# Performance work log

Hardware: AMD Instinct MI355X
Metric: run time of the kernel (lower is better)

## Reference

```python
import jax, jax.numpy as jnp
import numpy as np

STEPS_PER_PIECE = 4  # fixed-step RK4 substeps per spline piece (stands in for the adaptive solver)


def setup_inputs() -> dict:
    key = jax.random.key(0)
    ks = jax.random.split(key, 10)
    B, P, C, H, O = 4096, 64, 128, 128, 10  # batch, spline pieces, channels(=latent), hidden, output
    rn = lambda k, sh: jax.random.normal(k, sh, dtype=jnp.float32)
    return {
        "z0": rn(ks[0], (B, C)),
        # Hermite-cubic spline coefficients per piece: X(s) = a + b s + c s^2 + d s^3
        "coeffs": rn(ks[1], (B, P, C, 4)) * 0.05,
        "W1": rn(ks[2], (C, H)) / np.sqrt(C).astype(np.float32),
        "b1": jnp.zeros((H,), jnp.float32),
        "W2": rn(ks[3], (H, H)) / np.sqrt(H).astype(np.float32),
        "b2": jnp.zeros((H,), jnp.float32),
        "W3": rn(ks[4], (H, C)) / np.sqrt(H).astype(np.float32),
        "b3": jnp.zeros((C,), jnp.float32),
        "Wr": rn(ks[5], (H, O)) / np.sqrt(H).astype(np.float32),
        "br": jnp.zeros((O,), jnp.float32),
    }


def reference(z0, coeffs, W1, b1, W2, b2, W3, b3, Wr, br):
    P = coeffs.shape[1]
    n_steps = P * STEPS_PER_PIECE
    dt = jnp.float32(1.0 / STEPS_PER_PIECE)  # spline piece i covers t in [i, i+1]

    def dXdt(t):
        # derivative of the cubic spline at scalar time t -> [B, C]
        idx = jnp.clip(jnp.floor(t).astype(jnp.int32), 0, P - 1)
        s = t - idx.astype(t.dtype)
        c = jax.lax.dynamic_index_in_dim(coeffs, idx, axis=1, keepdims=False)  # [B, C, 4]
        return c[..., 1] + (2.0 * c[..., 2] + 3.0 * c[..., 3] * s) * s

    def f(z):
        # CDEFunc: Linear -> ELU -> Linear -> ReLU -> Linear
        h = jax.nn.elu(z @ W1 + b1)
        h = jax.nn.relu(h @ W2 + b2)
        return h @ W3 + b3

    def rk4_step(z, t):
        k1 = f(z) * dXdt(t)
        k2 = f(z + 0.5 * dt * k1) * dXdt(t + 0.5 * dt)
        k3 = f(z + 0.5 * dt * k2) * dXdt(t + 0.5 * dt)
        k4 = f(z + dt * k3) * dXdt(t + dt)
        z = z + (dt / 6.0) * (k1 + 2.0 * k2 + 2.0 * k3 + k4)
        return z, None

    ts = jnp.arange(n_steps, dtype=jnp.float32) * dt
    zT, _ = jax.lax.scan(rk4_step, z0, ts)  # terminal latent state = zt[:, 1]
    return zT @ Wr + br
```

## Files before the change

kernel.cpp:

```cpp
#include <hip/hip_runtime.h>
#include <hip/hip_bf16.h>
#include <math.h>


typedef short bf16x8 __attribute__((ext_vector_type(8)));
typedef float f32x4  __attribute__((ext_vector_type(4)));
typedef unsigned int u32x2 __attribute__((ext_vector_type(2)));

#define MFMA16(a, b, c) __builtin_amdgcn_mfma_f32_16x16x32_bf16((a), (b), (c), 0, 0, 0)

__device__ __forceinline__ unsigned short f2bf(float x) {
  unsigned int u = __float_as_uint(x);
  u += 0x7FFFu + ((u >> 16) & 1u);
  return (unsigned short)(u >> 16);
}

__device__ __forceinline__ unsigned int cvt_pk(float lo, float hi) {
  unsigned int r;
  asm("v_cvt_pk_bf16_f32 %0, %1, %2" : "=v"(r) : "v"(lo), "v"(hi));
  return r;
}

__device__ __forceinline__ void barrier_lgkm() {
  asm volatile("s_waitcnt lgkmcnt(0)" ::: "memory");
  __builtin_amdgcn_s_barrier();
  asm volatile("" ::: "memory");
}

__global__ __launch_bounds__(512, 2) void cde_fused(
    const float* __restrict__ z0, const float* __restrict__ coeffs,
    const float* __restrict__ W1, const float* __restrict__ b1,
    const float* __restrict__ W2, const float* __restrict__ b2,
    const float* __restrict__ W3, const float* __restrict__ b3,
    const float* __restrict__ Wr, const float* __restrict__ br,
    float* __restrict__ out) {
  __shared__ __align__(16) unsigned short zbuf[2][16][136];
  char* const lds = (char*)&zbuf[0][0][0];

  const int tid  = (int)threadIdx.x;
  const int lane = tid & 63;
  const int wv   = tid >> 6;
  const int l15  = lane & 15;
  const int q    = lane >> 4;
  const int n16  = wv * 16 + l15;
  const int nb4  = wv * 16 + q * 4;
  const int row0 = (int)blockIdx.x * 16;

  const int rdbyte = l15 * 272 + q * 16;
  const int wrbyte = l15 * 272 + nb4 * 2;

  bf16x8 wf1[4], wf2[4], wf3[4];
#pragma unroll
  for (int ks = 0; ks < 4; ++ks) {
    bf16x8 fa, fb, fc;
#pragma unroll
    for (int i = 0; i < 8; ++i) {
      const int k = ks * 32 + q * 8 + i;
      fa[i] = (short)f2bf(W1[k * 128 + n16]);
      fb[i] = (short)f2bf(W2[k * 128 + n16]);
      fc[i] = (short)f2bf(W3[k * 128 + n16]);
    }
    wf1[ks] = fa; wf2[ks] = fb; wf3[ks] = fc;
  }
  const f32x4 bv1 = *(const f32x4*)(b1 + nb4);
  const f32x4 bv2 = *(const f32x4*)(b2 + nb4);
  const f32x4 bv3 = *(const f32x4*)(b3 + nb4);

  f32x4 cf[4];
  auto coeff_load = [&](int p) {
    const float* cb = coeffs + ((size_t)(row0 + l15) * 64 + p) * 512 + nb4 * 4;
#pragma unroll
    for (int r = 0; r < 4; ++r) cf[r] = *(const f32x4*)(cb + r * 4);
  };
  float c1v[4], c2b[4], c3b[4];
  auto coeff_adopt = [&]() {
#pragma unroll
    for (int r = 0; r < 4; ++r) {
      c1v[r] = cf[r][1]; c2b[r] = 2.f * cf[r][2]; c3b[r] = 3.f * cf[r][3];
    }
  };

  auto stv = [&](int wb, const f32x4 v) {
    u32x2 w;
    w[0] = cvt_pk(v[0], v[1]);
    w[1] = cvt_pk(v[2], v[3]);
    *(u32x2*)(lds + (wb * 4352 + wrbyte)) = w;
  };

  float zr[4];
  {
    const f32x4 z = *(const f32x4*)(z0 + (size_t)(row0 + l15) * 128 + nb4);
#pragma unroll
    for (int r = 0; r < 4; ++r) zr[r] = z[r];
  }
  coeff_load(0);
  coeff_adopt();
  stv(0, f32x4{zr[0], zr[1], zr[2], zr[3]});
  barrier_lgkm();

  float kx[4], sacc[4], dxb[4];

  auto layer = [&](const bf16x8(&wf)[4], const f32x4 bias, int rb) -> f32x4 {
    const char* base = lds + rb * 4352 + rdbyte;
    bf16x8 x0 = *(const bf16x8*)(base);
    bf16x8 x1 = *(const bf16x8*)(base + 64);
    bf16x8 x2 = *(const bf16x8*)(base + 128);
    bf16x8 x3 = *(const bf16x8*)(base + 192);
    f32x4 Aa = {0.f, 0.f, 0.f, 0.f}, Ab = bias;
    Aa = MFMA16(wf[0], x0, Aa); Ab = MFMA16(wf[1], x1, Ab);
    Aa = MFMA16(wf[2], x2, Aa); Ab = MFMA16(wf[3], x3, Ab);
    return Aa + Ab;
  };

  auto run_f = [&](int sp) {
    f32x4 A = layer(wf1, bv1, sp);
    f32x4 h;
#pragma unroll
    for (int r = 0; r < 4; ++r) {
      const float v = A[r];
      h[r] = fmaxf(v, __expf(fminf(v, 0.f)) - 1.f);
    }
    stv(sp ^ 1, h);
    barrier_lgkm();
    A = layer(wf2, bv2, sp ^ 1);
#pragma unroll
    for (int r = 0; r < 4; ++r) h[r] = fmaxf(A[r], 0.f);
    stv(sp, h);
    barrier_lgkm();
    A = layer(wf3, bv3, sp);
#pragma unroll
    for (int r = 0; r < 4; ++r) kx[r] = A[r];
  };

#pragma unroll 1
  for (int p = 0; p < 64; ++p) {
    const bool pre = p < 63;
    if (pre) coeff_load(p + 1);

#pragma unroll
    for (int sub = 0; sub < 4; ++sub) {
      const float s0 = 0.25f * (float)sub;

      run_f(0);
      {
        f32x4 h;
#pragma unroll
        for (int r = 0; r < 4; ++r) {
          const float dx = c1v[r] + (c2b[r] + c3b[r] * s0) * s0;
          kx[r] *= dx; sacc[r] = kx[r];
          h[r] = zr[r] + 0.125f * kx[r];
        }
        stv(1, h);
      }
      barrier_lgkm();

      run_f(1);
      {
        const float sb = s0 + 0.125f;
        f32x4 h;
#pragma unroll
        for (int r = 0; r < 4; ++r) {
          dxb[r] = c1v[r] + (c2b[r] + c3b[r] * sb) * sb;
          kx[r] *= dxb[r]; sacc[r] += 2.f * kx[r];
          h[r] = zr[r] + 0.125f * kx[r];
        }
        stv(0, h);
      }
      barrier_lgkm();

      run_f(0);
      {
        f32x4 h;
#pragma unroll
        for (int r = 0; r < 4; ++r) {
          kx[r] *= dxb[r]; sacc[r] += 2.f * kx[r];
          h[r] = zr[r] + 0.25f * kx[r];
        }
        stv(1, h);
      }
      barrier_lgkm();

      run_f(1);
      if (sub == 3) {
        if (pre) {
#pragma unroll
          for (int r = 0; r < 4; ++r) kx[r] *= cf[r][1];
        } else {
#pragma unroll
          for (int r = 0; r < 4; ++r) kx[r] *= (c1v[r] + c2b[r] + c3b[r]);
        }
      } else {
        const float sc = s0 + 0.25f;
#pragma unroll
        for (int r = 0; r < 4; ++r)
          kx[r] *= c1v[r] + (c2b[r] + c3b[r] * sc) * sc;
      }
      {
        f32x4 h;
#pragma unroll
        for (int r = 0; r < 4; ++r) {
          sacc[r] += kx[r];
          zr[r] += (0.25f / 6.f) * sacc[r];
          h[r] = zr[r];
        }
        stv(0, h);
      }
      barrier_lgkm();
    }
    if (pre) coeff_adopt();
  }

  {
    float* zf = (float*)lds;
    *(f32x4*)(zf + l15 * 132 + nb4) = f32x4{zr[0], zr[1], zr[2], zr[3]};
  }
  barrier_lgkm();
  if (tid < 160) {
    const int row = tid / 10, o = tid - row * 10;
    const float* zf = (const float*)lds;
    float acc = br[o];
#pragma unroll 4
    for (int ch = 0; ch < 128; ++ch)
      acc = fmaf(zf[row * 132 + ch], Wr[ch * 10 + o], acc);
    out[(size_t)(row0 + row) * 10 + o] = acc;
  }
}

extern "C" void kernel_launch(void* const* d_in, const int* in_sizes, int n_in,
                              void* d_out, int out_size, void* d_ws, size_t ws_size,
                              hipStream_t stream) {
  const float* z0     = (const float*)d_in[0];
  const float* coeffs = (const float*)d_in[1];
  const float* W1 = (const float*)d_in[2]; const float* b1 = (const float*)d_in[3];
  const float* W2 = (const float*)d_in[4]; const float* b2 = (const float*)d_in[5];
  const float* W3 = (const float*)d_in[6]; const float* b3 = (const float*)d_in[7];
  const float* Wr = (const float*)d_in[8]; const float* br = (const float*)d_in[9];
  hipLaunchKernelGGL(cde_fused, dim3(256), dim3(512), 0, stream,
                     z0, coeffs, W1, b1, W2, b2, W3, b3, Wr, br, (float*)d_out);
}
```

Baseline: 823.4 us.

## Halve block to 4 waves, each computing two 16-column output tiles

Each wave now owns 32 output columns (two MFMA N-tiles) instead of 16, so the block shrinks from 8 to 4 waves. This halves the waves that take part in each of the many per-layer barriers, and each LDS activation fragment loaded feeds two MFMA chains, which raises instruction-level parallelism per wave. In exchange, per-wave register use doubles for weights and state. With 256 blocks on the GPU there may also be less latency hiding per CU.

```diff
diff --git a/kernel.cpp b/kernel.cpp
--- a/kernel.cpp
+++ b/kernel.cpp
@@ -27,7 +27,7 @@
   asm volatile("" ::: "memory");
 }
 
-__global__ __launch_bounds__(512, 2) void cde_fused(
+__global__ __launch_bounds__(256, 1) void cde_fused(
     const float* __restrict__ z0, const float* __restrict__ coeffs,
     const float* __restrict__ W1, const float* __restrict__ b1,
     const float* __restrict__ W2, const float* __restrict__ b2,
@@ -42,94 +42,118 @@
   const int wv   = tid >> 6;
   const int l15  = lane & 15;
   const int q    = lane >> 4;
-  const int n16  = wv * 16 + l15;
-  const int nb4  = wv * 16 + q * 4;
+  const int cb0  = wv * 32;
   const int row0 = (int)blockIdx.x * 16;
 
   const int rdbyte = l15 * 272 + q * 16;
-  const int wrbyte = l15 * 272 + nb4 * 2;
-
-  bf16x8 wf1[4], wf2[4], wf3[4];
-#pragma unroll
-  for (int ks = 0; ks < 4; ++ks) {
-    bf16x8 fa, fb, fc;
-#pragma unroll
-    for (int i = 0; i < 8; ++i) {
-      const int k = ks * 32 + q * 8 + i;
-      fa[i] = (short)f2bf(W1[k * 128 + n16]);
-      fb[i] = (short)f2bf(W2[k * 128 + n16]);
-      fc[i] = (short)f2bf(W3[k * 128 + n16]);
-    }
-    wf1[ks] = fa; wf2[ks] = fb; wf3[ks] = fc;
-  }
-  const f32x4 bv1 = *(const f32x4*)(b1 + nb4);
-  const f32x4 bv2 = *(const f32x4*)(b2 + nb4);
-  const f32x4 bv3 = *(const f32x4*)(b3 + nb4);
-
-  f32x4 cf[4];
+  const int wrbyte0 = l15 * 272 + (cb0 + 4 * q) * 2;
+  const int wrbyte1 = wrbyte0 + 32;
+
+  bf16x8 wf1[2][4], wf2[2][4], wf3[2][4];
+#pragma unroll
+  for (int mt = 0; mt < 2; ++mt) {
+    const int col = cb0 + 16 * mt + l15;
+#pragma unroll
+    for (int ks = 0; ks < 4; ++ks) {
+      bf16x8 fa, fb, fc;
+#pragma unroll
+      for (int i = 0; i < 8; ++i) {
+        const int k = ks * 32 + q * 8 + i;
+        fa[i] = (short)f2bf(W1[k * 128 + col]);
+        fb[i] = (short)f2bf(W2[k * 128 + col]);
+        fc[i] = (short)f2bf(W3[k * 128 + col]);
+      }
+      wf1[mt][ks] = fa; wf2[mt][ks] = fb; wf3[mt][ks] = fc;
+    }
+  }
+  f32x4 bv1[2], bv2[2], bv3[2];
+#pragma unroll
+  for (int mt = 0; mt < 2; ++mt) {
+    bv1[mt] = *(const f32x4*)(b1 + cb0 + 16 * mt + 4 * q);
+    bv2[mt] = *(const f32x4*)(b2 + cb0 + 16 * mt + 4 * q);
+    bv3[mt] = *(const f32x4*)(b3 + cb0 + 16 * mt + 4 * q);
+  }
+
+  f32x4 cf[8];
   auto coeff_load = [&](int p) {
-    const float* cb = coeffs + ((size_t)(row0 + l15) * 64 + p) * 512 + nb4 * 4;
-#pragma unroll
-    for (int r = 0; r < 4; ++r) cf[r] = *(const f32x4*)(cb + r * 4);
-  };
-  float c1v[4], c2b[4], c3b[4];
+    const float* cb = coeffs + ((size_t)(row0 + l15) * 64 + p) * 512;
+#pragma unroll
+    for (int mt = 0; mt < 2; ++mt)
+#pragma unroll
+      for (int r = 0; r < 4; ++r)
+        cf[mt * 4 + r] = *(const f32x4*)(cb + (cb0 + 16 * mt + 4 * q + r) * 4);
+  };
+  float c1v[8], c2b[8], c3b[8];
   auto coeff_adopt = [&]() {
 #pragma unroll
-    for (int r = 0; r < 4; ++r) {
-      c1v[r] = cf[r][1]; c2b[r] = 2.f * cf[r][2]; c3b[r] = 3.f * cf[r][3];
-    }
-  };
-
-  auto stv = [&](int wb, const f32x4 v) {
-    u32x2 w;
-    w[0] = cvt_pk(v[0], v[1]);
-    w[1] = cvt_pk(v[2], v[3]);
-    *(u32x2*)(lds + (wb * 4352 + wrbyte)) = w;
-  };
-
-  float zr[4];
+    for (int e = 0; e < 8; ++e) {
+      c1v[e] = cf[e][1]; c2b[e] = 2.f * cf[e][2]; c3b[e] = 3.f * cf[e][3];
+    }
+  };
+
+  auto stv = [&](int wb, const float (&h)[8]) {
+    u32x2 w0, w1;
+    w0[0] = cvt_pk(h[0], h[1]); w0[1] = cvt_pk(h[2], h[3]);
+    w1[0] = cvt_pk(h[4], h[5]); w1[1] = cvt_pk(h[6], h[7]);
+    *(u32x2*)(lds + (wb * 4352 + wrbyte0)) = w0;
+    *(u32x2*)(lds + (wb * 4352 + wrbyte1)) = w1;
+  };
+
+  float zr[8];
   {
-    const f32x4 z = *(const f32x4*)(z0 + (size_t)(row0 + l15) * 128 + nb4);
-#pragma unroll
-    for (int r = 0; r < 4; ++r) zr[r] = z[r];
+    const float* zp = z0 + (size_t)(row0 + l15) * 128;
+    const f32x4 za = *(const f32x4*)(zp + cb0 + 4 * q);
+    const f32x4 zb = *(const f32x4*)(zp + cb0 + 16 + 4 * q);
+#pragma unroll
+    for (int r = 0; r < 4; ++r) { zr[r] = za[r]; zr[4 + r] = zb[r]; }
   }
   coeff_load(0);
   coeff_adopt();
-  stv(0, f32x4{zr[0], zr[1], zr[2], zr[3]});
+  {
+    float h[8];
+#pragma unroll
+    for (int e = 0; e < 8; ++e) h[e] = zr[e];
+    stv(0, h);
+  }
   barrier_lgkm();
 
-  float kx[4], sacc[4], dxb[4];
-
-  auto layer = [&](const bf16x8(&wf)[4], const f32x4 bias, int rb) -> f32x4 {
+  float kx[8], sacc[8], dxb[8];
+
+  auto layer = [&](const bf16x8(&wf)[2][4], const f32x4(&bias)[2], int rb,
+                   f32x4& A0, f32x4& A1) {
     const char* base = lds + rb * 4352 + rdbyte;
     bf16x8 x0 = *(const bf16x8*)(base);
     bf16x8 x1 = *(const bf16x8*)(base + 64);
     bf16x8 x2 = *(const bf16x8*)(base + 128);
     bf16x8 x3 = *(const bf16x8*)(base + 192);
-    f32x4 Aa = {0.f, 0.f, 0.f, 0.f}, Ab = bias;
-    Aa = MFMA16(wf[0], x0, Aa); Ab = MFMA16(wf[1], x1, Ab);
-    Aa = MFMA16(wf[2], x2, Aa); Ab = MFMA16(wf[3], x3, Ab);
-    return Aa + Ab;
+    A0 = bias[0]; A1 = bias[1];
+    A0 = MFMA16(wf[0][0], x0, A0); A1 = MFMA16(wf[1][0], x0, A1);
+    A0 = MFMA16(wf[0][1], x1, A0); A1 = MFMA16(wf[1][1], x1, A1);
+    A0 = MFMA16(wf[0][2], x2, A0); A1 = MFMA16(wf[1][2], x2, A1);
+    A0 = MFMA16(wf[0][3], x3, A0); A1 = MFMA16(wf[1][3], x3, A1);
   };
 
   auto run_f = [&](int sp) {
-    f32x4 A = layer(wf1, bv1, sp);
-    f32x4 h;
+    f32x4 A0, A1;
+    float h[8];
+    layer(wf1, bv1, sp, A0, A1);
 #pragma unroll
     for (int r = 0; r < 4; ++r) {
-      const float v = A[r];
-      h[r] = fmaxf(v, __expf(fminf(v, 0.f)) - 1.f);
+      h[r]     = fmaxf(A0[r], __expf(fminf(A0[r], 0.f)) - 1.f);
+      h[4 + r] = fmaxf(A1[r], __expf(fminf(A1[r], 0.f)) - 1.f);
     }
     stv(sp ^ 1, h);
     barrier_lgkm();
-    A = layer(wf2, bv2, sp ^ 1);
-#pragma unroll
-    for (int r = 0; r < 4; ++r) h[r] = fmaxf(A[r], 0.f);
+    layer(wf2, bv2, sp ^ 1, A0, A1);
+#pragma unroll
+    for (int r = 0; r < 4; ++r) {
+      h[r] = fmaxf(A0[r], 0.f); h[4 + r] = fmaxf(A1[r], 0.f);
+    }
     stv(sp, h);
     barrier_lgkm();
-    A = layer(wf3, bv3, sp);
-#pragma unroll
-    for (int r = 0; r < 4; ++r) kx[r] = A[r];
+    layer(wf3, bv3, sp, A0, A1);
+#pragma unroll
+    for (int r = 0; r < 4; ++r) { kx[r] = A0[r]; kx[4 + r] = A1[r]; }
   };
 
 #pragma unroll 1
@@ -143,12 +167,12 @@
 
       run_f(0);
       {
-        f32x4 h;
-#pragma unroll
-        for (int r = 0; r < 4; ++r) {
-          const float dx = c1v[r] + (c2b[r] + c3b[r] * s0) * s0;
-          kx[r] *= dx; sacc[r] = kx[r];
-          h[r] = zr[r] + 0.125f * kx[r];
+        float h[8];
+#pragma unroll
+        for (int e = 0; e < 8; ++e) {
+          const float dx = c1v[e] + (c2b[e] + c3b[e] * s0) * s0;
+          kx[e] *= dx; sacc[e] = kx[e];
+          h[e] = zr[e] + 0.125f * kx[e];
         }
         stv(1, h);
       }
@@ -157,12 +181,12 @@
       run_f(1);
       {
         const float sb = s0 + 0.125f;
-        f32x4 h;
-#pragma unroll
-        for (int r = 0; r < 4; ++r) {
-          dxb[r] = c1v[r] + (c2b[r] + c3b[r] * sb) * sb;
-          kx[r] *= dxb[r]; sacc[r] += 2.f * kx[r];
-          h[r] = zr[r] + 0.125f * kx[r];
+        float h[8];
+#pragma unroll
+        for (int e = 0; e < 8; ++e) {
+          dxb[e] = c1v[e] + (c2b[e] + c3b[e] * sb) * sb;
+          kx[e] *= dxb[e]; sacc[e] += 2.f * kx[e];
+          h[e] = zr[e] + 0.125f * kx[e];
         }
         stv(0, h);
       }
@@ -170,11 +194,11 @@
 
       run_f(0);
       {
-        f32x4 h;
-#pragma unroll
-        for (int r = 0; r < 4; ++r) {
-          kx[r] *= dxb[r]; sacc[r] += 2.f * kx[r];
-          h[r] = zr[r] + 0.25f * kx[r];
+        float h[8];
+#pragma unroll
+        for (int e = 0; e < 8; ++e) {
+          kx[e] *= dxb[e]; sacc[e] += 2.f * kx[e];
+          h[e] = zr[e] + 0.25f * kx[e];
         }
         stv(1, h);
       }
@@ -184,24 +208,24 @@
       if (sub == 3) {
         if (pre) {
 #pragma unroll
-          for (int r = 0; r < 4; ++r) kx[r] *= cf[r][1];
+          for (int e = 0; e < 8; ++e) kx[e] *= cf[e][1];
         } else {
 #pragma unroll
-          for (int r = 0; r < 4; ++r) kx[r] *= (c1v[r] + c2b[r] + c3b[r]);
+          for (int e = 0; e < 8; ++e) kx[e] *= (c1v[e] + c2b[e] + c3b[e]);
         }
       } else {
         const float sc = s0 + 0.25f;
 #pragma unroll
-        for (int r = 0; r < 4; ++r)
-          kx[r] *= c1v[r] + (c2b[r] + c3b[r] * sc) * sc;
-      }
-      {
-        f32x4 h;
-#pragma unroll
-        for (int r = 0; r < 4; ++r) {
-          sacc[r] += kx[r];
-          zr[r] += (0.25f / 6.f) * sacc[r];
-          h[r] = zr[r];
+        for (int e = 0; e < 8; ++e)
+          kx[e] *= c1v[e] + (c2b[e] + c3b[e] * sc) * sc;
+      }
+      {
+        float h[8];
+#pragma unroll
+        for (int e = 0; e < 8; ++e) {
+          sacc[e] += kx[e];
+          zr[e] += (0.25f / 6.f) * sacc[e];
+          h[e] = zr[e];
         }
         stv(0, h);
       }
@@ -212,7 +236,8 @@
 
   {
     float* zf = (float*)lds;
-    *(f32x4*)(zf + l15 * 132 + nb4) = f32x4{zr[0], zr[1], zr[2], zr[3]};
+    *(f32x4*)(zf + l15 * 132 + cb0 + 4 * q)      = f32x4{zr[0], zr[1], zr[2], zr[3]};
+    *(f32x4*)(zf + l15 * 132 + cb0 + 16 + 4 * q) = f32x4{zr[4], zr[5], zr[6], zr[7]};
   }
   barrier_lgkm();
   if (tid < 160) {
@@ -235,6 +260,6 @@
   const float* W2 = (const float*)d_in[4]; const float* b2 = (const float*)d_in[5];
   const float* W3 = (const float*)d_in[6]; const float* b3 = (const float*)d_in[7];
   const float* Wr = (const float*)d_in[8]; const float* br = (const float*)d_in[9];
-  hipLaunchKernelGGL(cde_fused, dim3(256), dim3(512), 0, stream,
+  hipLaunchKernelGGL(cde_fused, dim3(256), dim3(256), 0, stream,
                      z0, coeffs, W1, b1, W2, b2, W3, b3, Wr, br, (float*)d_out);
 }
```

Result: faster. 804.8 us (-2.3%).
